# Performance work log

Measured on AMD Instinct MI355X. Metric: run time of the kernel, lower is better.

## Reference

```python
import jax, jax.numpy as jnp
import numpy as np

N, T, L = 4, 2048, 2048
DQIN, DFEAT, DQK, DV = 32, 34, 64, 64  # modality feat=34 -> V input = 34-2 = 32, K input = last col


def _sorted_timeline(k, shape):
    return jnp.sort(jax.random.uniform(k, shape, jnp.float32) * 100.0, axis=-1)


def setup_inputs() -> dict:
    key = jax.random.key(0)
    ks = jax.random.split(key, 32)
    inp = {}
    inp["ref_data"] = jax.random.normal(ks[0], (N, 1, T, DQIN), jnp.float32)
    inp["ref_t"] = _sorted_timeline(ks[1], (N, 1, T))
    inp["m1_data"] = jax.random.normal(ks[2], (N, 1, L, DFEAT), jnp.float32)
    inp["m1_t"] = _sorted_timeline(ks[3], (N, 1, L))
    inp["m2_data"] = jax.random.normal(ks[4], (N, 1, L, DFEAT), jnp.float32)
    inp["m2_t"] = _sorted_timeline(ks[5], (N, 1, L))
    inp["m3_data"] = jax.random.normal(ks[6], (N, 1, L, DFEAT), jnp.float32)
    inp["m3_t"] = _sorted_timeline(ks[7], (N, 1, L))
    # shared W_Q (bias=False): d_q_in -> d_qk
    inp["Wq"] = jax.random.normal(ks[8], (DQIN, DQK), jnp.float32) / np.sqrt(DQIN)
    # per-modality params: W_K: 1 -> d_qk (with bias), W_V: (DFEAT-2) -> d_v (with bias), log-temperature
    for i, m in enumerate(["1", "2", "3"]):
        b = 9 + 4 * i
        inp["Wk" + m] = jax.random.normal(ks[b], (1, DQK), jnp.float32)
        inp["bk" + m] = jax.random.normal(ks[b + 1], (DQK,), jnp.float32) * 0.02
        inp["Wv" + m] = jax.random.normal(ks[b + 2], (DFEAT - 2, DV), jnp.float32) / np.sqrt(DFEAT - 2)
        inp["bv" + m] = jax.random.normal(ks[b + 3], (DV,), jnp.float32) * 0.02
        inp["log_tau" + m] = jnp.zeros((), jnp.float32)  # log(init_tau=1)
    return inp


def _unimodal(Q, ref_t, data, t, Wk, bk, Wv, bv, log_tau):
    # K path: last feature column through linear, then feature_map_k = [1, -x]
    Kr = data[..., -1:] @ Wk + bk                                   # (N,1,L,DQK)
    K = jnp.concatenate([jnp.ones(Kr.shape[:-1] + (1,), Kr.dtype), -Kr], axis=-1)  # (N,1,L,DQK+1)
    V = data[..., :-2] @ Wv + bv                                    # (N,1,L,DV)
    tau = jnp.exp(log_tau)
    # gaussian weight: -(Q.K)^2 / tau
    S = -jnp.square(jnp.einsum('nhtc,nhlc->nhtl', Q, K)) / tau       # (N,1,T,L)
    mask = (ref_t[..., :, None] >= t[..., None, :]).astype(S.dtype)  # (N,1,T,L)
    A = jax.nn.softmax(S * mask, axis=-1) * mask
    return jnp.einsum('nhtl,nhlc->nhtc', A, V)                       # (N,1,T,DV)


def reference(ref_data, ref_t, m1_data, m1_t, m2_data, m2_t, m3_data, m3_t,
              Wq, Wk1, bk1, Wv1, bv1, log_tau1, Wk2, bk2, Wv2, bv2, log_tau2,
              Wk3, bk3, Wv3, bv3, log_tau3):
    # compute_Q (qk_type='time'): Q = add_one(W_Q(ref_data)) -> append ones column
    Qr = jnp.einsum('nhtd,dk->nhtk', ref_data, Wq)
    Q = jnp.concatenate([Qr, jnp.ones(Qr.shape[:-1] + (1,), Qr.dtype)], axis=-1)  # (N,1,T,DQK+1)
    y1 = _unimodal(Q, ref_t, m1_data, m1_t, Wk1, bk1, Wv1, bv1, log_tau1)
    y2 = _unimodal(Q, ref_t, m2_data, m2_t, Wk2, bk2, Wv2, bv2, log_tau2)
    y3 = _unimodal(Q, ref_t, m3_data, m3_t, Wk3, bk3, Wv3, bv3, log_tau3)
    # original returns dict {m1: y1, m2: y2, m3: y3}; stacked here (3,N,1,T,DV)
    return jnp.stack([y1, y2, y3], axis=0)
```

## Files before the change

### kernel.cpp

```cpp
#include <hip/hip_runtime.h>

namespace {

typedef unsigned int uint;
typedef unsigned short ushort_t;
typedef __attribute__((ext_vector_type(8))) short bf16x8;
typedef __attribute__((ext_vector_type(4))) float f32x4;

constexpr int N = 4, T = 2048, L = 2048;
constexpr int DQIN = 32, DQK = 64;

constexpr int VI_SZ = 3 * N * 64 * L;
constexpr int X_SZ = 3 * N * L;
constexpr int A_SZ = 3 * N * T;

union PK8 { int i[4]; bf16x8 s; };

__global__ __launch_bounds__(256) void mm_prep(
    const float* __restrict__ ref_data, const float* __restrict__ ref_t,
    const float* __restrict__ d1, const float* __restrict__ t1,
    const float* __restrict__ d2, const float* __restrict__ t2,
    const float* __restrict__ d3, const float* __restrict__ t3,
    const float* __restrict__ Wq,
    const float* __restrict__ Wk1, const float* __restrict__ bk1,
    const float* __restrict__ Wv1, const float* __restrict__ bv1, const float* __restrict__ lt1,
    const float* __restrict__ Wk2, const float* __restrict__ bk2,
    const float* __restrict__ Wv2, const float* __restrict__ bv2, const float* __restrict__ lt2,
    const float* __restrict__ Wk3, const float* __restrict__ bk3,
    const float* __restrict__ Wv3, const float* __restrict__ bv3, const float* __restrict__ lt3,
    float* __restrict__ Aq, float* __restrict__ Gq, int* __restrict__ Cq,
    ushort_t* __restrict__ VI, float* __restrict__ X) {
  const int b = blockIdx.x;
  const int tid = threadIdx.x;

  if (b < 32) {
    __shared__ float sWq[DQIN * DQK];
    __shared__ float sWk[3][DQK];
    __shared__ float sbk[3][DQK];
    for (int i = tid; i < DQIN * DQK; i += 256) sWq[i] = Wq[i];
    if (tid < DQK) {
      sWk[0][tid] = Wk1[tid]; sWk[1][tid] = Wk2[tid]; sWk[2][tid] = Wk3[tid];
      sbk[0][tid] = bk1[tid]; sbk[1][tid] = bk2[tid]; sbk[2][tid] = bk3[tid];
    }
    __syncthreads();
    const int idx = b * 256 + tid;
    float x[DQIN];
    const float* rp = ref_data + idx * DQIN;
#pragma unroll
    for (int i = 0; i < DQIN; i++) x[i] = rp[i];
    float qr[DQK];
#pragma unroll
    for (int j = 0; j < DQK; j += 4) {
      float4 acc4 = make_float4(0.f, 0.f, 0.f, 0.f);
#pragma unroll
      for (int i = 0; i < DQIN; i++) {
        const float4 w = *(const float4*)&sWq[i * DQK + j];
        acc4.x = fmaf(x[i], w.x, acc4.x);
        acc4.y = fmaf(x[i], w.y, acc4.y);
        acc4.z = fmaf(x[i], w.z, acc4.z);
        acc4.w = fmaf(x[i], w.w, acc4.w);
      }
      qr[j] = acc4.x; qr[j + 1] = acc4.y; qr[j + 2] = acc4.z; qr[j + 3] = acc4.w;
    }
    const float rs[3] = {__expf(-0.5f * lt1[0]), __expf(-0.5f * lt2[0]), __expf(-0.5f * lt3[0])};
#pragma unroll
    for (int m = 0; m < 3; m++) {
      float g = 0.f, h = 0.f;
#pragma unroll
      for (int j = 1; j < DQK; j++) {
        g = fmaf(qr[j], sWk[m][j - 1], g);
        h = fmaf(qr[j], sbk[m][j - 1], h);
      }
      g += sWk[m][DQK - 1];
      h += sbk[m][DQK - 1];
      Aq[m * (N * T) + idx] = (qr[0] - h) * rs[m];
      Gq[m * (N * T) + idx] = g * rs[m];
    }
  } else if (b < 128) {
    const int sidx = (b - 32) * 256 + tid;
    const int m = sidx >> 13;
    const int nt = sidx & 8191;
    const int n = nt >> 11;
    const float rt = ref_t[nt];
    const float* tml = ((m == 0) ? t1 : (m == 1 ? t2 : t3)) + n * L;
    int lo = 0, hi = L;
    while (lo < hi) {
      const int mid = (lo + hi) >> 1;
      if (tml[mid] <= rt) lo = mid + 1; else hi = mid;
    }
    Cq[m * 8192 + nt] = lo;
  } else {
    const int vb = b - 128;
    const int mn = vb >> 5;
    const int m = mn >> 2, n = mn & 3;
    const int lseg0 = (vb & 31) * 64;
    const float* dm = (m == 0) ? d1 : (m == 1 ? d2 : d3);
    const float* Wv = (m == 0) ? Wv1 : (m == 1 ? Wv2 : Wv3);
    const float* bv = (m == 0) ? bv1 : (m == 1 ? bv2 : bv3);
    const int cdim = tid & 63;
    const int qq = tid >> 6;
    const int l0 = lseg0 + qq * 16;

    float Wc[32];
#pragma unroll
    for (int i = 0; i < 32; i++) Wc[i] = Wv[i * 64 + cdim];
    const float bvc = bv[cdim];

    uint hi16[16], lo16[16];
#pragma unroll 4
    for (int k = 0; k < 16; k++) {
      const float* dp = dm + (size_t)(n * L + l0 + k) * 34;
      float acc = bvc;
#pragma unroll
      for (int i = 0; i < 32; i++) acc = fmaf(dp[i], Wc[i], acc);
      uint u = __float_as_uint(acc);
      uint h = (u + 0x7fffu + ((u >> 16) & 1u)) & 0xffff0000u;
      float res = acc - __uint_as_float(h);
      uint ul = __float_as_uint(res);
      uint hl = (ul + 0x7fffu + ((ul >> 16) & 1u)) >> 16;
      hi16[k] = h >> 16;
      lo16[k] = hl;
    }
    int pkh[8], pkl[8];
#pragma unroll
    for (int p = 0; p < 8; p++) {
      pkh[p] = (int)(hi16[2 * p] | (hi16[2 * p + 1] << 16));
      pkl[p] = (int)(lo16[2 * p] | (lo16[2 * p + 1] << 16));
    }
    ushort_t* dst = VI + (size_t)(mn * 64 + cdim) * (2 * L) + (l0 >> 3) * 16;
    *(int4*)dst = make_int4(pkh[0], pkh[1], pkh[2], pkh[3]);
    *(int4*)(dst + 8) = make_int4(pkl[0], pkl[1], pkl[2], pkl[3]);
    *(int4*)(dst + 16) = make_int4(pkh[4], pkh[5], pkh[6], pkh[7]);
    *(int4*)(dst + 24) = make_int4(pkl[4], pkl[5], pkl[6], pkl[7]);

    if (tid < 64) {
      const int l = lseg0 + tid;
      X[mn * L + l] = dm[(size_t)(n * L + l) * 34 + 33];
    }
  }
}

struct Buf {
  bf16x8 h[4];
  bf16x8 l[4];
  float4 x0, x1;
};

__device__ inline void load_buf(Buf& B, const ushort_t* vbase, const float* xp, int hc, int q) {
  const int p = hc * 4 + q;
#pragma unroll
  for (int ct = 0; ct < 4; ct++) {
    const ushort_t* ptr = vbase + (size_t)ct * (16 * 2 * L) + p * 16;
    B.h[ct] = *(const bf16x8*)ptr;
    B.l[ct] = *(const bf16x8*)(ptr + 8);
  }
  const int k0 = hc * 32 + q * 8;
  B.x0 = *(const float4*)&xp[k0];
  B.x1 = *(const float4*)&xp[k0 + 4];
}

__device__ inline void step(const Buf& B, int hc, int q, int c, int cmin,
                            float a, float g, f32x4 acc[4], float& z) {
  const int base = hc * 32;
  const int k0 = base + q * 8;
  const float xs[8] = {B.x0.x, B.x0.y, B.x0.z, B.x0.w, B.x1.x, B.x1.y, B.x1.z, B.x1.w};
  float w[8];
  if (base + 32 <= cmin) {
#pragma unroll
    for (int j = 0; j < 8; j++) {
      const float d = fmaf(-g, xs[j], a);
      w[j] = __expf(-d * d);
      z += w[j];
    }
  } else {
#pragma unroll
    for (int j = 0; j < 8; j++) {
      const float d = fmaf(-g, xs[j], a);
      const float e = __expf(-d * d);
      w[j] = (k0 + j < c) ? e : 0.f;
      z += w[j];
    }
  }
  PK8 ph, pl;
#pragma unroll
  for (int p2 = 0; p2 < 4; p2++) {
    const uint u0 = __float_as_uint(w[2 * p2]);
    const uint u1 = __float_as_uint(w[2 * p2 + 1]);
    const uint h0 = u0 & 0xffff0000u, h1 = u1 & 0xffff0000u;
    const float l0f = w[2 * p2] - __uint_as_float(h0);
    const float l1f = w[2 * p2 + 1] - __uint_as_float(h1);
    ph.i[p2] = (int)((h0 >> 16) | h1);
    pl.i[p2] = (int)((__float_as_uint(l0f) >> 16) | (__float_as_uint(l1f) & 0xffff0000u));
  }
  const bf16x8 ahi = ph.s, alo = pl.s;
#pragma unroll
  for (int ct = 0; ct < 4; ct++) {
    acc[ct] = __builtin_amdgcn_mfma_f32_16x16x32_bf16(ahi, B.h[ct], acc[ct], 0, 0, 0);
    acc[ct] = __builtin_amdgcn_mfma_f32_16x16x32_bf16(ahi, B.l[ct], acc[ct], 0, 0, 0);
    acc[ct] = __builtin_amdgcn_mfma_f32_16x16x32_bf16(alo, B.h[ct], acc[ct], 0, 0, 0);
  }
}

__global__ __launch_bounds__(256) void mm_attn_main(
    const ushort_t* __restrict__ VI, const float* __restrict__ X,
    const float* __restrict__ Aq, const float* __restrict__ Gq, const int* __restrict__ Cq,
    float* __restrict__ out) {
  __shared__ float sAcc[4][16][68];
  __shared__ float sZ[4][16];
  __shared__ int sC[16];

  const int b = blockIdx.x;
  const int mn = b % 12;
  const int r = b / 12;
  const int rg = (r & 1) ? (127 - (r >> 1)) : (r >> 1);
  const int tbase = mn * T + rg * 16;

  const int tid = threadIdx.x;
  const int lane = tid & 63;
  const int w = tid >> 6;
  const int q = lane >> 4;
  const int m16 = lane & 15;

  const int c = Cq[tbase + m16];
  const int cmax = __shfl(c, 15, 64);
  const int cmin = __shfl(c, 0, 64);
  const float a = Aq[tbase + m16];
  const float g = Gq[tbase + m16];

  if (tid < 16) sC[tid] = c;

  f32x4 acc[4];
#pragma unroll
  for (int ct = 0; ct < 4; ct++) acc[ct] = (f32x4){0.f, 0.f, 0.f, 0.f};
  float z = 0.f;

  const int nch = (cmax + 63) >> 6;
  const int s0 = (w * nch) >> 2;
  const int s1 = ((w + 1) * nch) >> 2;
  int hc = 2 * s0;
  const int hcE = 2 * s1;

  const ushort_t* vbase = VI + (size_t)(mn * 64 + m16) * (2 * L);
  const float* xp = X + mn * L;

  if (hc < hcE) {
    Buf A, B2;
    load_buf(A, vbase, xp, hc, q);
    for (; hc + 2 <= hcE; hc += 2) {
      load_buf(B2, vbase, xp, hc + 1, q);
      step(A, hc, q, c, cmin, a, g, acc, z);
      if (hc + 2 < hcE) load_buf(A, vbase, xp, hc + 2, q);
      step(B2, hc + 1, q, c, cmin, a, g, acc, z);
    }
    if (hc < hcE) step(A, hc, q, c, cmin, a, g, acc, z);
  }

  z += __shfl_xor(z, 16, 64);
  z += __shfl_xor(z, 32, 64);
  if (lane < 16) sZ[w][lane] = z;
#pragma unroll
  for (int ct = 0; ct < 4; ct++) {
#pragma unroll
    for (int rr = 0; rr < 4; rr++) {
      sAcc[w][q * 4 + rr][ct * 16 + m16] = acc[ct][rr];
    }
  }
  __syncthreads();

  const int row = tid >> 4;
  const int col = (tid & 15) * 4;
  float4 s0v = *(const float4*)&sAcc[0][row][col];
  const float4 s1v = *(const float4*)&sAcc[1][row][col];
  const float4 s2v = *(const float4*)&sAcc[2][row][col];
  const float4 s3v = *(const float4*)&sAcc[3][row][col];
  const float Zr = sZ[0][row] + sZ[1][row] + sZ[2][row] + sZ[3][row] + (float)(L - sC[row]);
  const float inv = 1.0f / Zr;
  s0v.x = (s0v.x + s1v.x + s2v.x + s3v.x) * inv;
  s0v.y = (s0v.y + s1v.y + s2v.y + s3v.y) * inv;
  s0v.z = (s0v.z + s1v.z + s2v.z + s3v.z) * inv;
  s0v.w = (s0v.w + s1v.w + s2v.w + s3v.w) * inv;
  *(float4*)&out[(size_t)(tbase + row) * 64 + col] = s0v;
}

}

extern "C" void kernel_launch(void* const* d_in, const int* in_sizes, int n_in,
                              void* d_out, int out_size, void* d_ws, size_t ws_size,
                              hipStream_t stream) {
  const float* ref_data = (const float*)d_in[0];
  const float* ref_t = (const float*)d_in[1];
  const float* m1_data = (const float*)d_in[2];
  const float* m1_t = (const float*)d_in[3];
  const float* m2_data = (const float*)d_in[4];
  const float* m2_t = (const float*)d_in[5];
  const float* m3_data = (const float*)d_in[6];
  const float* m3_t = (const float*)d_in[7];
  const float* Wq = (const float*)d_in[8];
  const float* Wk1 = (const float*)d_in[9];
  const float* bk1 = (const float*)d_in[10];
  const float* Wv1 = (const float*)d_in[11];
  const float* bv1 = (const float*)d_in[12];
  const float* lt1 = (const float*)d_in[13];
  const float* Wk2 = (const float*)d_in[14];
  const float* bk2 = (const float*)d_in[15];
  const float* Wv2 = (const float*)d_in[16];
  const float* bv2 = (const float*)d_in[17];
  const float* lt2 = (const float*)d_in[18];
  const float* Wk3 = (const float*)d_in[19];
  const float* bk3 = (const float*)d_in[20];
  const float* Wv3 = (const float*)d_in[21];
  const float* bv3 = (const float*)d_in[22];
  const float* lt3 = (const float*)d_in[23];

  float* ws = (float*)d_ws;
  ushort_t* VI = (ushort_t*)ws;
  float* Xw = ws + VI_SZ;
  float* Aq = Xw + X_SZ;
  float* Gq = Aq + A_SZ;
  int* Cq = (int*)(Gq + A_SZ);

  mm_prep<<<dim3(512), dim3(256), 0, stream>>>(
      ref_data, ref_t, m1_data, m1_t, m2_data, m2_t, m3_data, m3_t, Wq,
      Wk1, bk1, Wv1, bv1, lt1, Wk2, bk2, Wv2, bv2, lt2, Wk3, bk3, Wv3, bv3, lt3,
      Aq, Gq, Cq, VI, Xw);
  mm_attn_main<<<dim3(12 * 128), dim3(256), 0, stream>>>(
      VI, Xw, Aq, Gq, Cq, (float*)d_out);
}
```

Baseline: 178.9 us.

## Stage V chunks in LDS via async global_load_lds and split output columns across waves

Before, each wave took its own slice of the key dimension and loaded V straight from global into registers, then the four waves' partial accumulators were reduced through shared memory. Now each wave owns 16 output columns and all waves walk every key chunk. V chunks are staged into a double-buffered, swizzled LDS tile with direct global-to-LDS loads, which removes the cross-wave reduction. In exchange every wave recomputes the exp weights for all keys, adding about four times the exp work, and a block barrier runs on every chunk. The block scheduling order of row groups is also reversed.

```diff
diff --git a/kernel.cpp b/kernel.cpp
--- a/kernel.cpp
+++ b/kernel.cpp
@@ -140,64 +140,19 @@
   }
 }
 
-struct Buf {
-  bf16x8 h[4];
-  bf16x8 l[4];
-  float4 x0, x1;
-};
-
-__device__ inline void load_buf(Buf& B, const ushort_t* vbase, const float* xp, int hc, int q) {
-  const int p = hc * 4 + q;
-#pragma unroll
-  for (int ct = 0; ct < 4; ct++) {
-    const ushort_t* ptr = vbase + (size_t)ct * (16 * 2 * L) + p * 16;
-    B.h[ct] = *(const bf16x8*)ptr;
-    B.l[ct] = *(const bf16x8*)(ptr + 8);
-  }
-  const int k0 = hc * 32 + q * 8;
-  B.x0 = *(const float4*)&xp[k0];
-  B.x1 = *(const float4*)&xp[k0 + 4];
-}
-
-__device__ inline void step(const Buf& B, int hc, int q, int c, int cmin,
-                            float a, float g, f32x4 acc[4], float& z) {
-  const int base = hc * 32;
-  const int k0 = base + q * 8;
-  const float xs[8] = {B.x0.x, B.x0.y, B.x0.z, B.x0.w, B.x1.x, B.x1.y, B.x1.z, B.x1.w};
-  float w[8];
-  if (base + 32 <= cmin) {
-#pragma unroll
-    for (int j = 0; j < 8; j++) {
-      const float d = fmaf(-g, xs[j], a);
-      w[j] = __expf(-d * d);
-      z += w[j];
-    }
-  } else {
-#pragma unroll
-    for (int j = 0; j < 8; j++) {
-      const float d = fmaf(-g, xs[j], a);
-      const float e = __expf(-d * d);
-      w[j] = (k0 + j < c) ? e : 0.f;
-      z += w[j];
-    }
-  }
-  PK8 ph, pl;
-#pragma unroll
-  for (int p2 = 0; p2 < 4; p2++) {
-    const uint u0 = __float_as_uint(w[2 * p2]);
-    const uint u1 = __float_as_uint(w[2 * p2 + 1]);
-    const uint h0 = u0 & 0xffff0000u, h1 = u1 & 0xffff0000u;
-    const float l0f = w[2 * p2] - __uint_as_float(h0);
-    const float l1f = w[2 * p2 + 1] - __uint_as_float(h1);
-    ph.i[p2] = (int)((h0 >> 16) | h1);
-    pl.i[p2] = (int)((__float_as_uint(l0f) >> 16) | (__float_as_uint(l1f) & 0xffff0000u));
-  }
-  const bf16x8 ahi = ph.s, alo = pl.s;
-#pragma unroll
-  for (int ct = 0; ct < 4; ct++) {
-    acc[ct] = __builtin_amdgcn_mfma_f32_16x16x32_bf16(ahi, B.h[ct], acc[ct], 0, 0, 0);
-    acc[ct] = __builtin_amdgcn_mfma_f32_16x16x32_bf16(ahi, B.l[ct], acc[ct], 0, 0, 0);
-    acc[ct] = __builtin_amdgcn_mfma_f32_16x16x32_bf16(alo, B.h[ct], acc[ct], 0, 0, 0);
+__device__ inline void stage_chunk(ushort_t* dstbuf, const ushort_t* VIb, int ch,
+                                   int w, int lane) {
+#pragma unroll
+  for (int i = 0; i < 4; i++) {
+    const int u = w * 256 + i * 64 + lane;
+    const int rr = u >> 4;
+    const int gs = u & 15;
+    const int g = (gs - rr) & 15;
+    const ushort_t* src = VIb + (size_t)rr * 4096 + ch * 128 + g * 8;
+    __builtin_amdgcn_global_load_lds(
+        (const __attribute__((address_space(1))) void*)src,
+        (__attribute__((address_space(3))) void*)(dstbuf + (size_t)(w * 256 + i * 64) * 8),
+        16, 0, 0);
   }
 }
 
@@ -205,14 +160,12 @@
     const ushort_t* __restrict__ VI, const float* __restrict__ X,
     const float* __restrict__ Aq, const float* __restrict__ Gq, const int* __restrict__ Cq,
     float* __restrict__ out) {
-  __shared__ float sAcc[4][16][68];
-  __shared__ float sZ[4][16];
-  __shared__ int sC[16];
+  __shared__ ushort_t sbuf[2][8192];
 
   const int b = blockIdx.x;
   const int mn = b % 12;
   const int r = b / 12;
-  const int rg = (r & 1) ? (127 - (r >> 1)) : (r >> 1);
+  const int rg = (r & 1) ? (r >> 1) : (127 - (r >> 1));
   const int tbase = mn * T + rg * 16;
 
   const int tid = threadIdx.x;
@@ -224,62 +177,85 @@
   const int c = Cq[tbase + m16];
   const int cmax = __shfl(c, 15, 64);
   const int cmin = __shfl(c, 0, 64);
-  const float a = Aq[tbase + m16];
-  const float g = Gq[tbase + m16];
-
-  if (tid < 16) sC[tid] = c;
-
-  f32x4 acc[4];
-#pragma unroll
-  for (int ct = 0; ct < 4; ct++) acc[ct] = (f32x4){0.f, 0.f, 0.f, 0.f};
+  const int nch = (cmax + 63) >> 6;
+
+  float a = 0.f, g = 0.f;
+  if (nch > 0) { a = Aq[tbase + m16]; g = Gq[tbase + m16]; }
+
+  f32x4 acc = (f32x4){0.f, 0.f, 0.f, 0.f};
   float z = 0.f;
 
-  const int nch = (cmax + 63) >> 6;
-  const int s0 = (w * nch) >> 2;
-  const int s1 = ((w + 1) * nch) >> 2;
-  int hc = 2 * s0;
-  const int hcE = 2 * s1;
-
-  const ushort_t* vbase = VI + (size_t)(mn * 64 + m16) * (2 * L);
+  const ushort_t* VIb = VI + (size_t)mn * 64 * 4096;
   const float* xp = X + mn * L;
-
-  if (hc < hcE) {
-    Buf A, B2;
-    load_buf(A, vbase, xp, hc, q);
-    for (; hc + 2 <= hcE; hc += 2) {
-      load_buf(B2, vbase, xp, hc + 1, q);
-      step(A, hc, q, c, cmin, a, g, acc, z);
-      if (hc + 2 < hcE) load_buf(A, vbase, xp, hc + 2, q);
-      step(B2, hc + 1, q, c, cmin, a, g, acc, z);
-    }
-    if (hc < hcE) step(A, hc, q, c, cmin, a, g, acc, z);
+  const int rdim = w * 16 + m16;
+
+  if (nch > 0) stage_chunk(sbuf[0], VIb, 0, w, lane);
+  __syncthreads();
+
+  for (int ch = 0; ch < nch; ch++) {
+    const int nb = ch & 1;
+    if (ch + 1 < nch) stage_chunk(sbuf[nb ^ 1], VIb, ch + 1, w, lane);
+
+    const int base = ch << 6;
+    const ushort_t* buf = sbuf[nb];
+#pragma unroll
+    for (int hh = 0; hh < 2; hh++) {
+      const int k0 = base + hh * 32 + q * 8;
+      const float4 xa = *(const float4*)&xp[k0];
+      const float4 xb = *(const float4*)&xp[k0 + 4];
+      const float xs[8] = {xa.x, xa.y, xa.z, xa.w, xb.x, xb.y, xb.z, xb.w};
+      float wv[8];
+      if (base + hh * 32 + 32 <= cmin) {
+#pragma unroll
+        for (int j = 0; j < 8; j++) {
+          const float d = fmaf(-g, xs[j], a);
+          wv[j] = __expf(-d * d);
+          z += wv[j];
+        }
+      } else {
+#pragma unroll
+        for (int j = 0; j < 8; j++) {
+          const float d = fmaf(-g, xs[j], a);
+          const float e = __expf(-d * d);
+          wv[j] = (k0 + j < c) ? e : 0.f;
+          z += wv[j];
+        }
+      }
+      PK8 ph, pl;
+#pragma unroll
+      for (int p2 = 0; p2 < 4; p2++) {
+        const uint u0 = __float_as_uint(wv[2 * p2]);
+        const uint u1 = __float_as_uint(wv[2 * p2 + 1]);
+        const uint h0 = u0 & 0xffff0000u, h1 = u1 & 0xffff0000u;
+        const float l0f = wv[2 * p2] - __uint_as_float(h0);
+        const float l1f = wv[2 * p2 + 1] - __uint_as_float(h1);
+        ph.i[p2] = (int)((h0 >> 16) | h1);
+        pl.i[p2] = (int)((__float_as_uint(l0f) >> 16) | (__float_as_uint(l1f) & 0xffff0000u));
+      }
+      const bf16x8 ahi = ph.s, alo = pl.s;
+      const int g0 = (hh * 4 + q) * 2;
+      const int uih = rdim * 16 + ((g0 + rdim) & 15);
+      const int uil = rdim * 16 + ((g0 + 1 + rdim) & 15);
+      const bf16x8 bh = *(const bf16x8*)&buf[(size_t)uih * 8];
+      const bf16x8 bl = *(const bf16x8*)&buf[(size_t)uil * 8];
+      acc = __builtin_amdgcn_mfma_f32_16x16x32_bf16(ahi, bh, acc, 0, 0, 0);
+      acc = __builtin_amdgcn_mfma_f32_16x16x32_bf16(ahi, bl, acc, 0, 0, 0);
+      acc = __builtin_amdgcn_mfma_f32_16x16x32_bf16(alo, bh, acc, 0, 0, 0);
+    }
+    __syncthreads();
   }
 
   z += __shfl_xor(z, 16, 64);
   z += __shfl_xor(z, 32, 64);
-  if (lane < 16) sZ[w][lane] = z;
-#pragma unroll
-  for (int ct = 0; ct < 4; ct++) {
-#pragma unroll
-    for (int rr = 0; rr < 4; rr++) {
-      sAcc[w][q * 4 + rr][ct * 16 + m16] = acc[ct][rr];
-    }
+
+#pragma unroll
+  for (int rr2 = 0; rr2 < 4; rr2++) {
+    const int row = q * 4 + rr2;
+    const float zr = __shfl(z, row, 64);
+    const int cr = __shfl(c, row, 64);
+    const float inv = 1.0f / (zr + (float)(L - cr));
+    out[(size_t)(tbase + row) * 64 + w * 16 + m16] = acc[rr2] * inv;
   }
-  __syncthreads();
-
-  const int row = tid >> 4;
-  const int col = (tid & 15) * 4;
-  float4 s0v = *(const float4*)&sAcc[0][row][col];
-  const float4 s1v = *(const float4*)&sAcc[1][row][col];
-  const float4 s2v = *(const float4*)&sAcc[2][row][col];
-  const float4 s3v = *(const float4*)&sAcc[3][row][col];
-  const float Zr = sZ[0][row] + sZ[1][row] + sZ[2][row] + sZ[3][row] + (float)(L - sC[row]);
-  const float inv = 1.0f / Zr;
-  s0v.x = (s0v.x + s1v.x + s2v.x + s3v.x) * inv;
-  s0v.y = (s0v.y + s1v.y + s2v.y + s3v.y) * inv;
-  s0v.z = (s0v.z + s1v.z + s2v.z + s3v.z) * inv;
-  s0v.w = (s0v.w + s1v.w + s2v.w + s3v.w) * inv;
-  *(float4*)&out[(size_t)(tbase + row) * 64 + col] = s0v;
 }
 
 }
```

Measured after the change: 174.8 us. 2.3% less time.
